# Kernel optimization log

Hardware: AMD Instinct MI355X
Metric: run time of the kernel (lower is better)

Reference implementation:

```python
import jax, jax.numpy as jnp
import numpy as np

N, E = 50000, 800000
IN_DIM, HID, OUT, HEADS = 128, 128, 64, 4
C1 = HID // HEADS  # 32 per-head channels in gat1
NEG_SLOPE = 0.2


def _gat_conv(x, src, dst, W, a_src, a_dst, b, heads, ch):
    """PyG GATConv (inference): gather -> edge attention -> segment softmax -> scatter."""
    n = x.shape[0]
    h = (x @ W).reshape(n, heads, ch)                      # [N,H,C]
    alpha_src = jnp.einsum('nhc,hc->nh', h, a_src)         # [N,H]
    alpha_dst = jnp.einsum('nhc,hc->nh', h, a_dst)         # [N,H]
    e = jax.nn.leaky_relu(alpha_src[src] + alpha_dst[dst], NEG_SLOPE)  # [E,H]
    m = jax.ops.segment_max(e, dst, num_segments=n)        # per-target max (stable softmax)
    e = jnp.exp(e - m[dst])
    denom = jax.ops.segment_sum(e, dst, num_segments=n)
    alpha = e / (denom[dst] + 1e-16)                       # [E,H]
    out = jax.ops.segment_sum(h[src] * alpha[:, :, None], dst, num_segments=n)  # [N,H,C]
    return out.reshape(n, heads * ch) + b


def setup_inputs() -> dict:
    key = jax.random.key(0)
    ks = jax.random.split(key, 16)
    x = jax.random.normal(ks[0], (N, IN_DIM), dtype=jnp.float32)
    edge_index = jax.random.randint(ks[1], (2, E), 0, N, dtype=jnp.int64)
    s = lambda fan_in: 1.0 / np.sqrt(fan_in)
    return {
        'x': x,
        'edge_index': edge_index,
        'W1': jax.random.normal(ks[2], (IN_DIM, HEADS * C1), jnp.float32) * s(IN_DIM),
        'a_src1': jax.random.normal(ks[3], (HEADS, C1), jnp.float32) * s(C1),
        'a_dst1': jax.random.normal(ks[4], (HEADS, C1), jnp.float32) * s(C1),
        'b1': jnp.zeros((HID,), jnp.float32),
        'W2': jax.random.normal(ks[5], (HID, OUT), jnp.float32) * s(HID),
        'a_src2': jax.random.normal(ks[6], (1, OUT), jnp.float32) * s(OUT),
        'a_dst2': jax.random.normal(ks[7], (1, OUT), jnp.float32) * s(OUT),
        'b2': jnp.zeros((OUT,), jnp.float32),
        'pw1': jax.random.normal(ks[8], (OUT, OUT), jnp.float32) * s(OUT),
        'pb1': jnp.zeros((OUT,), jnp.float32),
        'pw2': jax.random.normal(ks[9], (OUT, OUT), jnp.float32) * s(OUT),
        'pb2': jnp.zeros((OUT,), jnp.float32),
    }


def reference(x, edge_index, W1, a_src1, a_dst1, b1, W2, a_src2, a_dst2, b2, pw1, pb1, pw2, pb2):
    n = x.shape[0]
    # PyG GATConv add_self_loops=True
    loops = jnp.arange(n, dtype=edge_index.dtype)
    src = jnp.concatenate([edge_index[0], loops])
    dst = jnp.concatenate([edge_index[1], loops])
    h = jax.nn.elu(_gat_conv(x, src, dst, W1, a_src1, a_dst1, b1, HEADS, C1))
    h = jax.nn.elu(_gat_conv(h, src, dst, W2, a_src2, a_dst2, b2, 1, OUT))
    # origin_proj: Linear -> ReLU -> Linear
    h = jax.nn.relu(h @ pw1 + pb1)
    return h @ pw2 + pb2
```

## Files before the change

### kernel.cpp

```cpp
#include <hip/hip_runtime.h>
#include <math.h>

#define N_NODES 50000
#define N_EDGES 800000
#define ET (N_EDGES + N_NODES)
#define IN_DIM 128
#define HID 128
#define OUT_DIM 64
#define BW 64
#define NBUCK ((N_NODES + BW - 1) / BW)
#define NBLK 256
#define EPB 3328

typedef __attribute__((ext_vector_type(8))) short bf16x8;
typedef __attribute__((ext_vector_type(4))) float f32x4;

__device__ __forceinline__ float lrelu(float x){ return x >= 0.f ? x : 0.2f * x; }
__device__ __forceinline__ float eluf(float x){ return x > 0.f ? x : expm1f(x); }
__device__ __forceinline__ unsigned f2bf(float f){
    unsigned u = __float_as_uint(f);
    return (u + 0x7fffu + ((u >> 16) & 1u)) >> 16;
}
__device__ __forceinline__ float bflo(unsigned u){ return __uint_as_float(u << 16); }
__device__ __forceinline__ float bfhi(unsigned u){ return __uint_as_float(u & 0xffff0000u); }

__global__ __launch_bounds__(256) void k_count(const int* __restrict__ dst, int* __restrict__ C)
{
    __shared__ int cnt[NBUCK];
    const int tid = threadIdx.x, blk = blockIdx.x;
    for (int i = tid; i < NBUCK; i += 256) cnt[i] = 0;
    __syncthreads();
    #pragma unroll
    for (int j = 0; j < EPB / 256; j++) {
        const int e = blk * EPB + j * 256 + tid;
        if (e < ET) {
            const int d = (e < N_EDGES) ? dst[e] : (e - N_EDGES);
            atomicAdd(&cnt[d >> 6], 1);
        }
    }
    __syncthreads();
    for (int b = tid; b < NBUCK; b += 256) C[b * NBLK + blk] = cnt[b];
}

__global__ __launch_bounds__(256) void k_bsumA(const int* __restrict__ C, int* __restrict__ bsum2)
{
    __shared__ int red[4];
    int v = C[blockIdx.x * NBLK + threadIdx.x];
    #pragma unroll
    for (int off = 32; off > 0; off >>= 1) v += __shfl_down(v, off);
    if ((threadIdx.x & 63) == 0) red[threadIdx.x >> 6] = v;
    __syncthreads();
    if (threadIdx.x == 0) bsum2[blockIdx.x] = red[0] + red[1] + red[2] + red[3];
}

__global__ __launch_bounds__(1024) void k_bscanB(const int* __restrict__ bsum2, int* __restrict__ boff2)
{
    __shared__ int part[1024];
    const int t = threadIdx.x;
    int v = (t < NBUCK) ? bsum2[t] : 0;
    part[t] = v;
    __syncthreads();
    #pragma unroll
    for (int d = 1; d < 1024; d <<= 1) {
        int add = (t >= d) ? part[t - d] : 0;
        __syncthreads();
        part[t] += add;
        __syncthreads();
    }
    if (t < NBUCK) boff2[t] = part[t] - v;
    if (t == 0) boff2[NBUCK] = ET;
}

__global__ __launch_bounds__(256) void k_cscanC(const int* __restrict__ C,
                                                const int* __restrict__ boff2,
                                                int* __restrict__ Cs)
{
    __shared__ int part[256];
    const int t = threadIdx.x, b = blockIdx.x;
    int v = C[b * NBLK + t];
    part[t] = v;
    __syncthreads();
    #pragma unroll
    for (int d = 1; d < 256; d <<= 1) {
        int add = (t >= d) ? part[t - d] : 0;
        __syncthreads();
        part[t] += add;
        __syncthreads();
    }
    Cs[b * NBLK + t] = boff2[b] + part[t] - v;
}

__global__ __launch_bounds__(256) void k_part2(const int* __restrict__ src,
                                               const int* __restrict__ dst,
                                               const int* __restrict__ Cs,
                                               uint2* __restrict__ part)
{
    __shared__ int base[NBUCK];
    __shared__ int cnt[NBUCK];
    const int tid = threadIdx.x, blk = blockIdx.x;
    for (int b = tid; b < NBUCK; b += 256) { base[b] = Cs[b * NBLK + blk]; cnt[b] = 0; }
    __syncthreads();
    #pragma unroll
    for (int j = 0; j < EPB / 256; j++) {
        const int e = blk * EPB + j * 256 + tid;
        if (e < ET) {
            int s, d;
            if (e < N_EDGES) { s = src[e]; d = dst[e]; } else { s = d = e - N_EDGES; }
            const int b = d >> 6;
            const int r = atomicAdd(&cnt[b], 1);
            part[base[b] + r] = make_uint2((unsigned)d, (unsigned)s);
        }
    }
}

__global__ __launch_bounds__(256) void k_scat2(const int* __restrict__ boff2,
                                               const uint2* __restrict__ part,
                                               int* __restrict__ rowptr,
                                               int* __restrict__ csr_src)
{
    __shared__ int cnt64[BW];
    __shared__ int nbase[BW];
    const int b = blockIdx.x, tid = threadIdx.x;
    const int n0 = b * BW;
    const int lo = boff2[b], hi = boff2[b + 1];
    if (tid < BW) cnt64[tid] = 0;
    __syncthreads();
    for (int i = lo + tid; i < hi; i += 256) {
        atomicAdd(&cnt64[part[i].x & (BW - 1)], 1);
    }
    __syncthreads();
    if (tid < BW) {
        int v = cnt64[tid];
        int incl = v;
        #pragma unroll
        for (int off = 1; off < 64; off <<= 1) {
            int t2 = __shfl_up(incl, off);
            if (tid >= off) incl += t2;
        }
        const int excl = incl - v;
        nbase[tid] = excl;
        const int n = n0 + tid;
        if (n < N_NODES) rowptr[n] = lo + excl;
        cnt64[tid] = 0;
    }
    if (b == 0 && tid == 0) rowptr[N_NODES] = ET;
    __syncthreads();
    for (int i = lo + tid; i < hi; i += 256) {
        const uint2 p = part[i];
        const int dn = (int)p.x & (BW - 1);
        const int r = atomicAdd(&cnt64[dn], 1);
        csr_src[lo + nbase[dn] + r] = (int)p.y;
    }
}

__global__ __launch_bounds__(256, 2) void k_gemm1(
    const float* __restrict__ x, const float* __restrict__ W1,
    const float* __restrict__ a_s, const float* __restrict__ a_d,
    unsigned* __restrict__ h1b, float* __restrict__ as1, float* __restrict__ ad1)
{
    __shared__ unsigned sWt[128 * 68];
    __shared__ unsigned sxb[64 * 68];
    const int tid = threadIdx.x;
    const int wave = tid >> 6;
    const int lane = tid & 63;
    const int ll   = lane & 15;
    const int quad = lane >> 4;
    const int n0 = blockIdx.x * 64;

    for (int idx = tid; idx < 8192; idx += 256) {
        const int n = idx & 127, kp = idx >> 7;
        const float w0 = W1[(2 * kp) * 128 + n];
        const float w1 = W1[(2 * kp + 1) * 128 + n];
        sWt[n * 68 + kp] = f2bf(w0) | (f2bf(w1) << 16);
    }
    for (int idx = tid; idx < 4096; idx += 256) {
        const int node = idx >> 6, kp = idx & 63;
        const int n = n0 + node;
        unsigned pk = 0;
        if (n < N_NODES) {
            const float x0 = x[n * 128 + 2 * kp];
            const float x1 = x[n * 128 + 2 * kp + 1];
            pk = f2bf(x0) | (f2bf(x1) << 16);
        }
        sxb[node * 68 + kp] = pk;
    }
    __syncthreads();

    f32x4 acc[8];
    #pragma unroll
    for (int t = 0; t < 8; t++) acc[t] = (f32x4){0.f, 0.f, 0.f, 0.f};

    #pragma unroll
    for (int kk = 0; kk < 4; kk++) {
        const int kpo = 16 * kk + 4 * quad;
        const bf16x8 a = *(const bf16x8*)&sxb[(16 * wave + ll) * 68 + kpo];
        #pragma unroll
        for (int t = 0; t < 8; t++) {
            const bf16x8 b = *(const bf16x8*)&sWt[(16 * t + ll) * 68 + kpo];
            acc[t] = __builtin_amdgcn_mfma_f32_16x16x32_bf16(a, b, acc[t], 0, 0, 0);
        }
    }

    float as_v[8], ad_v[8];
    #pragma unroll
    for (int t = 0; t < 8; t++) { as_v[t] = a_s[16 * t + ll]; ad_v[t] = a_d[16 * t + ll]; }
    unsigned short* h1u = (unsigned short*)h1b;
    #pragma unroll
    for (int r = 0; r < 4; r++) {
        const int n = n0 + 16 * wave + 4 * quad + r;
        float ps0 = acc[0][r] * as_v[0] + acc[1][r] * as_v[1];
        float ps1 = acc[2][r] * as_v[2] + acc[3][r] * as_v[3];
        float ps2 = acc[4][r] * as_v[4] + acc[5][r] * as_v[5];
        float ps3 = acc[6][r] * as_v[6] + acc[7][r] * as_v[7];
        float pd0 = acc[0][r] * ad_v[0] + acc[1][r] * ad_v[1];
        float pd1 = acc[2][r] * ad_v[2] + acc[3][r] * ad_v[3];
        float pd2 = acc[4][r] * ad_v[4] + acc[5][r] * ad_v[5];
        float pd3 = acc[6][r] * ad_v[6] + acc[7][r] * ad_v[7];
        #pragma unroll
        for (int off = 1; off < 16; off <<= 1) {
            ps0 += __shfl_xor(ps0, off); ps1 += __shfl_xor(ps1, off);
            ps2 += __shfl_xor(ps2, off); ps3 += __shfl_xor(ps3, off);
            pd0 += __shfl_xor(pd0, off); pd1 += __shfl_xor(pd1, off);
            pd2 += __shfl_xor(pd2, off); pd3 += __shfl_xor(pd3, off);
        }
        if (n < N_NODES) {
            #pragma unroll
            for (int t = 0; t < 8; t++)
                h1u[n * 128 + 16 * t + ll] = (unsigned short)f2bf(acc[t][r]);
            if (ll == 0) {
                as1[n * 4 + 0] = ps0; as1[n * 4 + 1] = ps1;
                as1[n * 4 + 2] = ps2; as1[n * 4 + 3] = ps3;
                ad1[n * 4 + 0] = pd0; ad1[n * 4 + 1] = pd1;
                ad1[n * 4 + 2] = pd2; ad1[n * 4 + 3] = pd3;
            }
        }
    }
}

__global__ __launch_bounds__(256) void k_aggr1(
    const int* __restrict__ rowptr, const int* __restrict__ csr_src,
    const float* __restrict__ as1, const float* __restrict__ ad1,
    const uint4* __restrict__ h1u4, float* __restrict__ acc1)
{
    const int d  = blockIdx.x * 16 + (threadIdx.x >> 4);
    const int c8 = threadIdx.x & 15;
    const int hd = c8 >> 2;
    const int r0 = rowptr[d], r1 = rowptr[d + 1];
    const float adv = ad1[d * 4 + hd];
    float den = 0.f;
    float acc[8];
    #pragma unroll
    for (int m = 0; m < 8; m++) acc[m] = 0.f;
    int i = r0;
    for (; i + 2 <= r1; i += 2) {
        const int s0 = csr_src[i], s1 = csr_src[i + 1];
        const float e0 = as1[s0 * 4 + hd], e1 = as1[s1 * 4 + hd];
        const uint4 u0 = h1u4[s0 * 16 + c8];
        const uint4 u1 = h1u4[s1 * 16 + c8];
        const float w0 = expf(lrelu(e0 + adv));
        const float w1 = expf(lrelu(e1 + adv));
        den += w0 + w1;
        acc[0] = fmaf(bflo(u0.x), w0, acc[0]); acc[1] = fmaf(bfhi(u0.x), w0, acc[1]);
        acc[2] = fmaf(bflo(u0.y), w0, acc[2]); acc[3] = fmaf(bfhi(u0.y), w0, acc[3]);
        acc[4] = fmaf(bflo(u0.z), w0, acc[4]); acc[5] = fmaf(bfhi(u0.z), w0, acc[5]);
        acc[6] = fmaf(bflo(u0.w), w0, acc[6]); acc[7] = fmaf(bfhi(u0.w), w0, acc[7]);
        acc[0] = fmaf(bflo(u1.x), w1, acc[0]); acc[1] = fmaf(bfhi(u1.x), w1, acc[1]);
        acc[2] = fmaf(bflo(u1.y), w1, acc[2]); acc[3] = fmaf(bfhi(u1.y), w1, acc[3]);
        acc[4] = fmaf(bflo(u1.z), w1, acc[4]); acc[5] = fmaf(bfhi(u1.z), w1, acc[5]);
        acc[6] = fmaf(bflo(u1.w), w1, acc[6]); acc[7] = fmaf(bfhi(u1.w), w1, acc[7]);
    }
    if (i < r1) {
        const int s = csr_src[i];
        const float w = expf(lrelu(as1[s * 4 + hd] + adv));
        const uint4 u = h1u4[s * 16 + c8];
        den += w;
        acc[0] = fmaf(bflo(u.x), w, acc[0]); acc[1] = fmaf(bfhi(u.x), w, acc[1]);
        acc[2] = fmaf(bflo(u.y), w, acc[2]); acc[3] = fmaf(bfhi(u.y), w, acc[3]);
        acc[4] = fmaf(bflo(u.z), w, acc[4]); acc[5] = fmaf(bfhi(u.z), w, acc[5]);
        acc[6] = fmaf(bflo(u.w), w, acc[6]); acc[7] = fmaf(bfhi(u.w), w, acc[7]);
    }
    const float inv = 1.f / (den + 1e-16f);
    float4 o0 = make_float4(acc[0] * inv, acc[1] * inv, acc[2] * inv, acc[3] * inv);
    float4 o1 = make_float4(acc[4] * inv, acc[5] * inv, acc[6] * inv, acc[7] * inv);
    ((float4*)acc1)[d * 32 + 2 * c8 + 0] = o0;
    ((float4*)acc1)[d * 32 + 2 * c8 + 1] = o1;
}

__global__ __launch_bounds__(256, 4) void k_layer2(
    const float* __restrict__ acc1, const float* __restrict__ b1,
    const float* __restrict__ W2, const float* __restrict__ a_s2, const float* __restrict__ a_d2,
    unsigned* __restrict__ h2b, float* __restrict__ as2, float* __restrict__ ad2)
{
    __shared__ unsigned sWt[64 * 68];
    __shared__ unsigned sxb[64 * 68];
    const int tid = threadIdx.x;
    const int wave = tid >> 6;
    const int lane = tid & 63;
    const int ll   = lane & 15;
    const int quad = lane >> 4;
    const int n0 = blockIdx.x * 64;

    for (int idx = tid; idx < 4096; idx += 256) {
        const int n = idx & 63, kp = idx >> 6;
        const float w0 = W2[(2 * kp) * 64 + n];
        const float w1 = W2[(2 * kp + 1) * 64 + n];
        sWt[n * 68 + kp] = f2bf(w0) | (f2bf(w1) << 16);
    }
    for (int idx = tid; idx < 4096; idx += 256) {
        const int node = idx >> 6, kp = idx & 63;
        const int n = n0 + node;
        unsigned pk = 0;
        if (n < N_NODES) {
            const float v0 = eluf(acc1[n * 128 + 2 * kp]     + b1[2 * kp]);
            const float v1 = eluf(acc1[n * 128 + 2 * kp + 1] + b1[2 * kp + 1]);
            pk = f2bf(v0) | (f2bf(v1) << 16);
        }
        sxb[node * 68 + kp] = pk;
    }
    __syncthreads();

    f32x4 acc[4];
    #pragma unroll
    for (int t = 0; t < 4; t++) acc[t] = (f32x4){0.f, 0.f, 0.f, 0.f};

    #pragma unroll
    for (int kk = 0; kk < 4; kk++) {
        const int kpo = 16 * kk + 4 * quad;
        const bf16x8 a = *(const bf16x8*)&sxb[(16 * wave + ll) * 68 + kpo];
        #pragma unroll
        for (int t = 0; t < 4; t++) {
            const bf16x8 b = *(const bf16x8*)&sWt[(16 * t + ll) * 68 + kpo];
            acc[t] = __builtin_amdgcn_mfma_f32_16x16x32_bf16(a, b, acc[t], 0, 0, 0);
        }
    }

    float as_v[4], ad_v[4];
    #pragma unroll
    for (int t = 0; t < 4; t++) { as_v[t] = a_s2[16 * t + ll]; ad_v[t] = a_d2[16 * t + ll]; }
    unsigned short* h2u = (unsigned short*)h2b;
    #pragma unroll
    for (int r = 0; r < 4; r++) {
        const int n = n0 + 16 * wave + 4 * quad + r;
        float ps = acc[0][r] * as_v[0] + acc[1][r] * as_v[1]
                 + acc[2][r] * as_v[2] + acc[3][r] * as_v[3];
        float pd = acc[0][r] * ad_v[0] + acc[1][r] * ad_v[1]
                 + acc[2][r] * ad_v[2] + acc[3][r] * ad_v[3];
        #pragma unroll
        for (int off = 1; off < 16; off <<= 1) {
            ps += __shfl_xor(ps, off);
            pd += __shfl_xor(pd, off);
        }
        if (n < N_NODES) {
            #pragma unroll
            for (int t = 0; t < 4; t++)
                h2u[n * 64 + 16 * t + ll] = (unsigned short)f2bf(acc[t][r]);
            if (ll == 0) { as2[n] = ps; ad2[n] = pd; }
        }
    }
}

__global__ __launch_bounds__(256) void k_aggr2(
    const int* __restrict__ rowptr, const int* __restrict__ csr_src,
    const float* __restrict__ as2, const float* __restrict__ ad2,
    const uint4* __restrict__ h2u4, float* __restrict__ acc2)
{
    const int d  = blockIdx.x * 32 + (threadIdx.x >> 3);
    const int c8 = threadIdx.x & 7;
    if (d >= N_NODES) return;
    const int r0 = rowptr[d], r1 = rowptr[d + 1];
    const float adv = ad2[d];
    float den = 0.f;
    float acc[8];
    #pragma unroll
    for (int m = 0; m < 8; m++) acc[m] = 0.f;
    int i = r0;
    for (; i + 2 <= r1; i += 2) {
        const int s0 = csr_src[i], s1 = csr_src[i + 1];
        const float e0 = as2[s0], e1 = as2[s1];
        const uint4 u0 = h2u4[s0 * 8 + c8];
        const uint4 u1 = h2u4[s1 * 8 + c8];
        const float w0 = expf(lrelu(e0 + adv));
        const float w1 = expf(lrelu(e1 + adv));
        den += w0 + w1;
        acc[0] = fmaf(bflo(u0.x), w0, acc[0]); acc[1] = fmaf(bfhi(u0.x), w0, acc[1]);
        acc[2] = fmaf(bflo(u0.y), w0, acc[2]); acc[3] = fmaf(bfhi(u0.y), w0, acc[3]);
        acc[4] = fmaf(bflo(u0.z), w0, acc[4]); acc[5] = fmaf(bfhi(u0.z), w0, acc[5]);
        acc[6] = fmaf(bflo(u0.w), w0, acc[6]); acc[7] = fmaf(bfhi(u0.w), w0, acc[7]);
        acc[0] = fmaf(bflo(u1.x), w1, acc[0]); acc[1] = fmaf(bfhi(u1.x), w1, acc[1]);
        acc[2] = fmaf(bflo(u1.y), w1, acc[2]); acc[3] = fmaf(bfhi(u1.y), w1, acc[3]);
        acc[4] = fmaf(bflo(u1.z), w1, acc[4]); acc[5] = fmaf(bfhi(u1.z), w1, acc[5]);
        acc[6] = fmaf(bflo(u1.w), w1, acc[6]); acc[7] = fmaf(bfhi(u1.w), w1, acc[7]);
    }
    if (i < r1) {
        const int s = csr_src[i];
        const float w = expf(lrelu(as2[s] + adv));
        const uint4 u = h2u4[s * 8 + c8];
        den += w;
        acc[0] = fmaf(bflo(u.x), w, acc[0]); acc[1] = fmaf(bfhi(u.x), w, acc[1]);
        acc[2] = fmaf(bflo(u.y), w, acc[2]); acc[3] = fmaf(bfhi(u.y), w, acc[3]);
        acc[4] = fmaf(bflo(u.z), w, acc[4]); acc[5] = fmaf(bfhi(u.z), w, acc[5]);
        acc[6] = fmaf(bflo(u.w), w, acc[6]); acc[7] = fmaf(bfhi(u.w), w, acc[7]);
    }
    const float inv = 1.f / (den + 1e-16f);
    float4 o0 = make_float4(acc[0] * inv, acc[1] * inv, acc[2] * inv, acc[3] * inv);
    float4 o1 = make_float4(acc[4] * inv, acc[5] * inv, acc[6] * inv, acc[7] * inv);
    ((float4*)acc2)[d * 16 + 2 * c8 + 0] = o0;
    ((float4*)acc2)[d * 16 + 2 * c8 + 1] = o1;
}

__global__ __launch_bounds__(256, 2) void k_out(
    const float* __restrict__ acc2, const float* __restrict__ b2,
    const float* __restrict__ pw1, const float* __restrict__ pb1,
    const float* __restrict__ pw2, const float* __restrict__ pb2,
    float* __restrict__ out)
{
    __shared__ float s1[64 * 64];
    __shared__ float s2[64 * 64];
    __shared__ float so[64][68];
    __shared__ float sp[64][68];
    const int tid = threadIdx.x;
    for (int i = tid; i < 1024; i += 256) {
        ((float4*)s1)[i] = ((const float4*)pw1)[i];
        ((float4*)s2)[i] = ((const float4*)pw2)[i];
    }
    const int cg = tid & 15;
    const int ng = tid >> 4;
    const float4 pb1_4 = ((const float4*)pb1)[cg];
    const float4 pb2_4 = ((const float4*)pb2)[cg];
    const int nGroups = (N_NODES + 63) / 64;
    for (int g = blockIdx.x; g < nGroups; g += gridDim.x) {
        const int n0 = g * 64;
        __syncthreads();
        #pragma unroll
        for (int j = 0; j < 4; j++) {
            const int i = tid + 256 * j;
            const int node = i >> 4, quad = i & 15;
            const int n = n0 + node;
            float4 v = make_float4(0.f, 0.f, 0.f, 0.f);
            if (n < N_NODES) {
                v = ((const float4*)acc2)[n * 16 + quad];
                const float4 bb = ((const float4*)b2)[quad];
                v.x = eluf(v.x + bb.x);
                v.y = eluf(v.y + bb.y);
                v.z = eluf(v.z + bb.z);
                v.w = eluf(v.w + bb.w);
            }
            *(float4*)&so[node][4 * quad] = v;
        }
        __syncthreads();
        float4 p[4];
        #pragma unroll
        for (int m = 0; m < 4; m++) p[m] = pb1_4;
        #pragma unroll 8
        for (int k = 0; k < 64; k++) {
            const float4 w = *(const float4*)&s1[k * 64 + 4 * cg];
            #pragma unroll
            for (int m = 0; m < 4; m++) {
                const float xv = so[4 * ng + m][k];
                p[m].x = fmaf(xv, w.x, p[m].x);
                p[m].y = fmaf(xv, w.y, p[m].y);
                p[m].z = fmaf(xv, w.z, p[m].z);
                p[m].w = fmaf(xv, w.w, p[m].w);
            }
        }
        #pragma unroll
        for (int m = 0; m < 4; m++) {
            p[m].x = fmaxf(p[m].x, 0.f); p[m].y = fmaxf(p[m].y, 0.f);
            p[m].z = fmaxf(p[m].z, 0.f); p[m].w = fmaxf(p[m].w, 0.f);
            *(float4*)&sp[4 * ng + m][4 * cg] = p[m];
        }
        __syncthreads();
        float4 o[4];
        #pragma unroll
        for (int m = 0; m < 4; m++) o[m] = pb2_4;
        #pragma unroll 8
        for (int k = 0; k < 64; k++) {
            const float4 w = *(const float4*)&s2[k * 64 + 4 * cg];
            #pragma unroll
            for (int m = 0; m < 4; m++) {
                const float xv = sp[4 * ng + m][k];
                o[m].x = fmaf(xv, w.x, o[m].x);
                o[m].y = fmaf(xv, w.y, o[m].y);
                o[m].z = fmaf(xv, w.z, o[m].z);
                o[m].w = fmaf(xv, w.w, o[m].w);
            }
        }
        #pragma unroll
        for (int m = 0; m < 4; m++) {
            const int n = n0 + 4 * ng + m;
            if (n < N_NODES) ((float4*)out)[n * 16 + cg] = o[m];
        }
    }
}

extern "C" void kernel_launch(void* const* d_in, const int* in_sizes, int n_in,
                              void* d_out, int out_size, void* d_ws, size_t ws_size,
                              hipStream_t stream)
{
    const float* x      = (const float*)d_in[0];
    const int*   ei     = (const int*)d_in[1];
    const int*   src    = ei;
    const int*   dst    = ei + N_EDGES;
    const float* W1     = (const float*)d_in[2];
    const float* a_src1 = (const float*)d_in[3];
    const float* a_dst1 = (const float*)d_in[4];
    const float* b1     = (const float*)d_in[5];
    const float* W2     = (const float*)d_in[6];
    const float* a_src2 = (const float*)d_in[7];
    const float* a_dst2 = (const float*)d_in[8];
    const float* b2     = (const float*)d_in[9];
    const float* pw1    = (const float*)d_in[10];
    const float* pb1    = (const float*)d_in[11];
    const float* pw2    = (const float*)d_in[12];
    const float* pb2    = (const float*)d_in[13];

    uint2* part  = (uint2*)d_ws;
    int* ibase   = (int*)(part + ET);
    int* rowptr  = ibase;
    int* C       = rowptr + 50001;
    int* Cs      = C + 200192;
    int* bsum2   = Cs + 200192;
    int* boff2   = bsum2 + 782;
    int* csr_src = boff2 + 785;
    unsigned* h1b = (unsigned*)(csr_src + 850000);
    unsigned* h2b = h1b + 3200000;
    float* fws   = (float*)(h2b + 1600000);
    float* as1   = fws;
    float* ad1   = as1 + 200000;
    float* acc1  = ad1 + 200000;
    float* as2   = acc1 + 6400000;
    float* ad2   = as2 + 50000;
    float* acc2  = ad2 + 50000;

    k_count<<<NBLK, 256, 0, stream>>>(dst, C);
    k_bsumA<<<NBUCK, 256, 0, stream>>>(C, bsum2);
    k_bscanB<<<1, 1024, 0, stream>>>(bsum2, boff2);
    k_cscanC<<<NBUCK, 256, 0, stream>>>(C, boff2, Cs);
    k_part2<<<NBLK, 256, 0, stream>>>(src, dst, Cs, part);
    k_scat2<<<NBUCK, 256, 0, stream>>>(boff2, part, rowptr, csr_src);

    k_gemm1<<<(N_NODES + 63) / 64, 256, 0, stream>>>(x, W1, a_src1, a_dst1, h1b, as1, ad1);
    k_aggr1<<<N_NODES / 16, 256, 0, stream>>>(rowptr, csr_src, as1, ad1,
                                              (const uint4*)h1b, acc1);

    k_layer2<<<(N_NODES + 63) / 64, 256, 0, stream>>>(acc1, b1, W2, a_src2, a_dst2, h2b, as2, ad2);
    k_aggr2<<<(N_NODES + 31) / 32, 256, 0, stream>>>(rowptr, csr_src, as2, ad2,
                                                     (const uint4*)h2b, acc2);

    k_out<<<782, 256, 0, stream>>>(acc2, b2, pw1, pb1, pw2, pb2, (float*)d_out);
}
```

Baseline: 247.2 us.

## Fuse GAT aggregation kernels into the following dense transform kernels

Merges layer-1 aggregation with the layer-2 GEMM, and layer-2 aggregation with the output MLP. Each block aggregates its 64 nodes straight into shared memory before the matmul, so the fp32 acc1 and acc2 intermediates no longer go to and from global memory and two launches disappear. In exchange each block now does a longer, irregular gather phase with less parallelism per node (16 or 8 threads loop over 4 or 2 nodes). This may reduce latency hiding, and the new launch bounds of 2 blocks per CU could limit occupancy.

```diff
diff --git a/kernel.cpp b/kernel.cpp
--- a/kernel.cpp
+++ b/kernel.cpp
@@ -237,67 +237,16 @@
     }
 }
 
-__global__ __launch_bounds__(256) void k_aggr1(
+__global__ __launch_bounds__(256, 2) void k_aggr1l2(
     const int* __restrict__ rowptr, const int* __restrict__ csr_src,
     const float* __restrict__ as1, const float* __restrict__ ad1,
-    const uint4* __restrict__ h1u4, float* __restrict__ acc1)
-{
-    const int d  = blockIdx.x * 16 + (threadIdx.x >> 4);
-    const int c8 = threadIdx.x & 15;
-    const int hd = c8 >> 2;
-    const int r0 = rowptr[d], r1 = rowptr[d + 1];
-    const float adv = ad1[d * 4 + hd];
-    float den = 0.f;
-    float acc[8];
-    #pragma unroll
-    for (int m = 0; m < 8; m++) acc[m] = 0.f;
-    int i = r0;
-    for (; i + 2 <= r1; i += 2) {
-        const int s0 = csr_src[i], s1 = csr_src[i + 1];
-        const float e0 = as1[s0 * 4 + hd], e1 = as1[s1 * 4 + hd];
-        const uint4 u0 = h1u4[s0 * 16 + c8];
-        const uint4 u1 = h1u4[s1 * 16 + c8];
-        const float w0 = expf(lrelu(e0 + adv));
-        const float w1 = expf(lrelu(e1 + adv));
-        den += w0 + w1;
-        acc[0] = fmaf(bflo(u0.x), w0, acc[0]); acc[1] = fmaf(bfhi(u0.x), w0, acc[1]);
-        acc[2] = fmaf(bflo(u0.y), w0, acc[2]); acc[3] = fmaf(bfhi(u0.y), w0, acc[3]);
-        acc[4] = fmaf(bflo(u0.z), w0, acc[4]); acc[5] = fmaf(bfhi(u0.z), w0, acc[5]);
-        acc[6] = fmaf(bflo(u0.w), w0, acc[6]); acc[7] = fmaf(bfhi(u0.w), w0, acc[7]);
-        acc[0] = fmaf(bflo(u1.x), w1, acc[0]); acc[1] = fmaf(bfhi(u1.x), w1, acc[1]);
-        acc[2] = fmaf(bflo(u1.y), w1, acc[2]); acc[3] = fmaf(bfhi(u1.y), w1, acc[3]);
-        acc[4] = fmaf(bflo(u1.z), w1, acc[4]); acc[5] = fmaf(bfhi(u1.z), w1, acc[5]);
-        acc[6] = fmaf(bflo(u1.w), w1, acc[6]); acc[7] = fmaf(bfhi(u1.w), w1, acc[7]);
-    }
-    if (i < r1) {
-        const int s = csr_src[i];
-        const float w = expf(lrelu(as1[s * 4 + hd] + adv));
-        const uint4 u = h1u4[s * 16 + c8];
-        den += w;
-        acc[0] = fmaf(bflo(u.x), w, acc[0]); acc[1] = fmaf(bfhi(u.x), w, acc[1]);
-        acc[2] = fmaf(bflo(u.y), w, acc[2]); acc[3] = fmaf(bfhi(u.y), w, acc[3]);
-        acc[4] = fmaf(bflo(u.z), w, acc[4]); acc[5] = fmaf(bfhi(u.z), w, acc[5]);
-        acc[6] = fmaf(bflo(u.w), w, acc[6]); acc[7] = fmaf(bfhi(u.w), w, acc[7]);
-    }
-    const float inv = 1.f / (den + 1e-16f);
-    float4 o0 = make_float4(acc[0] * inv, acc[1] * inv, acc[2] * inv, acc[3] * inv);
-    float4 o1 = make_float4(acc[4] * inv, acc[5] * inv, acc[6] * inv, acc[7] * inv);
-    ((float4*)acc1)[d * 32 + 2 * c8 + 0] = o0;
-    ((float4*)acc1)[d * 32 + 2 * c8 + 1] = o1;
-}
-
-__global__ __launch_bounds__(256, 4) void k_layer2(
-    const float* __restrict__ acc1, const float* __restrict__ b1,
+    const uint4* __restrict__ h1u4, const float* __restrict__ b1,
     const float* __restrict__ W2, const float* __restrict__ a_s2, const float* __restrict__ a_d2,
     unsigned* __restrict__ h2b, float* __restrict__ as2, float* __restrict__ ad2)
 {
     __shared__ unsigned sWt[64 * 68];
     __shared__ unsigned sxb[64 * 68];
     const int tid = threadIdx.x;
-    const int wave = tid >> 6;
-    const int lane = tid & 63;
-    const int ll   = lane & 15;
-    const int quad = lane >> 4;
     const int n0 = blockIdx.x * 64;
 
     for (int idx = tid; idx < 4096; idx += 256) {
@@ -306,23 +255,64 @@
         const float w1 = W2[(2 * kp + 1) * 64 + n];
         sWt[n * 68 + kp] = f2bf(w0) | (f2bf(w1) << 16);
     }
-    for (int idx = tid; idx < 4096; idx += 256) {
-        const int node = idx >> 6, kp = idx & 63;
-        const int n = n0 + node;
-        unsigned pk = 0;
-        if (n < N_NODES) {
-            const float v0 = eluf(acc1[n * 128 + 2 * kp]     + b1[2 * kp]);
-            const float v1 = eluf(acc1[n * 128 + 2 * kp + 1] + b1[2 * kp + 1]);
-            pk = f2bf(v0) | (f2bf(v1) << 16);
-        }
-        sxb[node * 68 + kp] = pk;
-    }
-    __syncthreads();
-
-    f32x4 acc[4];
-    #pragma unroll
-    for (int t = 0; t < 4; t++) acc[t] = (f32x4){0.f, 0.f, 0.f, 0.f};
-
+
+    const int g16 = tid >> 4;
+    const int c8  = tid & 15;
+    const int hd  = c8 >> 2;
+    for (int rep = 0; rep < 4; rep++) {
+        const int node = 4 * g16 + rep;
+        const int d = n0 + node;
+        float den = 0.f;
+        float acc[8];
+        #pragma unroll
+        for (int m = 0; m < 8; m++) acc[m] = 0.f;
+        if (d < N_NODES) {
+            const int r0 = rowptr[d], r1 = rowptr[d + 1];
+            const float adv = ad1[d * 4 + hd];
+            int i = r0;
+            for (; i + 2 <= r1; i += 2) {
+                const int s0 = csr_src[i], s1 = csr_src[i + 1];
+                const float e0 = as1[s0 * 4 + hd], e1 = as1[s1 * 4 + hd];
+                const uint4 u0 = h1u4[s0 * 16 + c8];
+                const uint4 u1 = h1u4[s1 * 16 + c8];
+                const float w0 = expf(lrelu(e0 + adv));
+                const float w1 = expf(lrelu(e1 + adv));
+                den += w0 + w1;
+                acc[0] = fmaf(bflo(u0.x), w0, acc[0]); acc[1] = fmaf(bfhi(u0.x), w0, acc[1]);
+                acc[2] = fmaf(bflo(u0.y), w0, acc[2]); acc[3] = fmaf(bfhi(u0.y), w0, acc[3]);
+                acc[4] = fmaf(bflo(u0.z), w0, acc[4]); acc[5] = fmaf(bfhi(u0.z), w0, acc[5]);
+                acc[6] = fmaf(bflo(u0.w), w0, acc[6]); acc[7] = fmaf(bfhi(u0.w), w0, acc[7]);
+                acc[0] = fmaf(bflo(u1.x), w1, acc[0]); acc[1] = fmaf(bfhi(u1.x), w1, acc[1]);
+                acc[2] = fmaf(bflo(u1.y), w1, acc[2]); acc[3] = fmaf(bfhi(u1.y), w1, acc[3]);
+                acc[4] = fmaf(bflo(u1.z), w1, acc[4]); acc[5] = fmaf(bfhi(u1.z), w1, acc[5]);
+                acc[6] = fmaf(bflo(u1.w), w1, acc[6]); acc[7] = fmaf(bfhi(u1.w), w1, acc[7]);
+            }
+            if (i < r1) {
+                const int s = csr_src[i];
+                const float w = expf(lrelu(as1[s * 4 + hd] + adv));
+                const uint4 u = h1u4[s * 16 + c8];
+                den += w;
+                acc[0] = fmaf(bflo(u.x), w, acc[0]); acc[1] = fmaf(bfhi(u.x), w, acc[1]);
+                acc[2] = fmaf(bflo(u.y), w, acc[2]); acc[3] = fmaf(bfhi(u.y), w, acc[3]);
+                acc[4] = fmaf(bflo(u.z), w, acc[4]); acc[5] = fmaf(bfhi(u.z), w, acc[5]);
+                acc[6] = fmaf(bflo(u.w), w, acc[6]); acc[7] = fmaf(bfhi(u.w), w, acc[7]);
+            }
+        }
+        const float inv = 1.f / (den + 1e-16f);
+        #pragma unroll
+        for (int j = 0; j < 4; j++) {
+            const float v0 = eluf(acc[2 * j]     * inv + b1[8 * c8 + 2 * j]);
+            const float v1 = eluf(acc[2 * j + 1] * inv + b1[8 * c8 + 2 * j + 1]);
+            sxb[node * 68 + 4 * c8 + j] = f2bf(v0) | (f2bf(v1) << 16);
+        }
+    }
+    __syncthreads();
+
+    const int wave = tid >> 6, lane = tid & 63;
+    const int ll = lane & 15, quad = lane >> 4;
+    f32x4 accm[4];
+    #pragma unroll
+    for (int t = 0; t < 4; t++) accm[t] = (f32x4){0.f, 0.f, 0.f, 0.f};
     #pragma unroll
     for (int kk = 0; kk < 4; kk++) {
         const int kpo = 16 * kk + 4 * quad;
@@ -330,10 +320,9 @@
         #pragma unroll
         for (int t = 0; t < 4; t++) {
             const bf16x8 b = *(const bf16x8*)&sWt[(16 * t + ll) * 68 + kpo];
-            acc[t] = __builtin_amdgcn_mfma_f32_16x16x32_bf16(a, b, acc[t], 0, 0, 0);
-        }
-    }
-
+            accm[t] = __builtin_amdgcn_mfma_f32_16x16x32_bf16(a, b, accm[t], 0, 0, 0);
+        }
+    }
     float as_v[4], ad_v[4];
     #pragma unroll
     for (int t = 0; t < 4; t++) { as_v[t] = a_s2[16 * t + ll]; ad_v[t] = a_d2[16 * t + ll]; }
@@ -341,10 +330,10 @@
     #pragma unroll
     for (int r = 0; r < 4; r++) {
         const int n = n0 + 16 * wave + 4 * quad + r;
-        float ps = acc[0][r] * as_v[0] + acc[1][r] * as_v[1]
-                 + acc[2][r] * as_v[2] + acc[3][r] * as_v[3];
-        float pd = acc[0][r] * ad_v[0] + acc[1][r] * ad_v[1]
-                 + acc[2][r] * ad_v[2] + acc[3][r] * ad_v[3];
+        float ps = accm[0][r] * as_v[0] + accm[1][r] * as_v[1]
+                 + accm[2][r] * as_v[2] + accm[3][r] * as_v[3];
+        float pd = accm[0][r] * ad_v[0] + accm[1][r] * ad_v[1]
+                 + accm[2][r] * ad_v[2] + accm[3][r] * ad_v[3];
         #pragma unroll
         for (int off = 1; off < 16; off <<= 1) {
             ps += __shfl_xor(ps, off);
@@ -353,63 +342,16 @@
         if (n < N_NODES) {
             #pragma unroll
             for (int t = 0; t < 4; t++)
-                h2u[n * 64 + 16 * t + ll] = (unsigned short)f2bf(acc[t][r]);
+                h2u[n * 64 + 16 * t + ll] = (unsigned short)f2bf(accm[t][r]);
             if (ll == 0) { as2[n] = ps; ad2[n] = pd; }
         }
     }
 }
 
-__global__ __launch_bounds__(256) void k_aggr2(
+__global__ __launch_bounds__(256, 2) void k_aggr2out(
     const int* __restrict__ rowptr, const int* __restrict__ csr_src,
     const float* __restrict__ as2, const float* __restrict__ ad2,
-    const uint4* __restrict__ h2u4, float* __restrict__ acc2)
-{
-    const int d  = blockIdx.x * 32 + (threadIdx.x >> 3);
-    const int c8 = threadIdx.x & 7;
-    if (d >= N_NODES) return;
-    const int r0 = rowptr[d], r1 = rowptr[d + 1];
-    const float adv = ad2[d];
-    float den = 0.f;
-    float acc[8];
-    #pragma unroll
-    for (int m = 0; m < 8; m++) acc[m] = 0.f;
-    int i = r0;
-    for (; i + 2 <= r1; i += 2) {
-        const int s0 = csr_src[i], s1 = csr_src[i + 1];
-        const float e0 = as2[s0], e1 = as2[s1];
-        const uint4 u0 = h2u4[s0 * 8 + c8];
-        const uint4 u1 = h2u4[s1 * 8 + c8];
-        const float w0 = expf(lrelu(e0 + adv));
-        const float w1 = expf(lrelu(e1 + adv));
-        den += w0 + w1;
-        acc[0] = fmaf(bflo(u0.x), w0, acc[0]); acc[1] = fmaf(bfhi(u0.x), w0, acc[1]);
-        acc[2] = fmaf(bflo(u0.y), w0, acc[2]); acc[3] = fmaf(bfhi(u0.y), w0, acc[3]);
-        acc[4] = fmaf(bflo(u0.z), w0, acc[4]); acc[5] = fmaf(bfhi(u0.z), w0, acc[5]);
-        acc[6] = fmaf(bflo(u0.w), w0, acc[6]); acc[7] = fmaf(bfhi(u0.w), w0, acc[7]);
-        acc[0] = fmaf(bflo(u1.x), w1, acc[0]); acc[1] = fmaf(bfhi(u1.x), w1, acc[1]);
-        acc[2] = fmaf(bflo(u1.y), w1, acc[2]); acc[3] = fmaf(bfhi(u1.y), w1, acc[3]);
-        acc[4] = fmaf(bflo(u1.z), w1, acc[4]); acc[5] = fmaf(bfhi(u1.z), w1, acc[5]);
-        acc[6] = fmaf(bflo(u1.w), w1, acc[6]); acc[7] = fmaf(bfhi(u1.w), w1, acc[7]);
-    }
-    if (i < r1) {
-        const int s = csr_src[i];
-        const float w = expf(lrelu(as2[s] + adv));
-        const uint4 u = h2u4[s * 8 + c8];
-        den += w;
-        acc[0] = fmaf(bflo(u.x), w, acc[0]); acc[1] = fmaf(bfhi(u.x), w, acc[1]);
-        acc[2] = fmaf(bflo(u.y), w, acc[2]); acc[3] = fmaf(bfhi(u.y), w, acc[3]);
-        acc[4] = fmaf(bflo(u.z), w, acc[4]); acc[5] = fmaf(bfhi(u.z), w, acc[5]);
-        acc[6] = fmaf(bflo(u.w), w, acc[6]); acc[7] = fmaf(bfhi(u.w), w, acc[7]);
-    }
-    const float inv = 1.f / (den + 1e-16f);
-    float4 o0 = make_float4(acc[0] * inv, acc[1] * inv, acc[2] * inv, acc[3] * inv);
-    float4 o1 = make_float4(acc[4] * inv, acc[5] * inv, acc[6] * inv, acc[7] * inv);
-    ((float4*)acc2)[d * 16 + 2 * c8 + 0] = o0;
-    ((float4*)acc2)[d * 16 + 2 * c8 + 1] = o1;
-}
-
-__global__ __launch_bounds__(256, 2) void k_out(
-    const float* __restrict__ acc2, const float* __restrict__ b2,
+    const uint4* __restrict__ h2u4, const float* __restrict__ b2,
     const float* __restrict__ pw1, const float* __restrict__ pb1,
     const float* __restrict__ pw2, const float* __restrict__ pb2,
     float* __restrict__ out)
@@ -419,77 +361,105 @@
     __shared__ float so[64][68];
     __shared__ float sp[64][68];
     const int tid = threadIdx.x;
+    const int n0 = blockIdx.x * 64;
     for (int i = tid; i < 1024; i += 256) {
         ((float4*)s1)[i] = ((const float4*)pw1)[i];
         ((float4*)s2)[i] = ((const float4*)pw2)[i];
     }
+
+    const int g8 = tid >> 3;
+    const int c8 = tid & 7;
+    for (int rep = 0; rep < 2; rep++) {
+        const int node = 2 * g8 + rep;
+        const int d = n0 + node;
+        float den = 0.f;
+        float acc[8];
+        #pragma unroll
+        for (int m = 0; m < 8; m++) acc[m] = 0.f;
+        if (d < N_NODES) {
+            const int r0 = rowptr[d], r1 = rowptr[d + 1];
+            const float adv = ad2[d];
+            int i = r0;
+            for (; i + 2 <= r1; i += 2) {
+                const int s0 = csr_src[i], s1v = csr_src[i + 1];
+                const float e0 = as2[s0], e1 = as2[s1v];
+                const uint4 u0 = h2u4[s0 * 8 + c8];
+                const uint4 u1 = h2u4[s1v * 8 + c8];
+                const float w0 = expf(lrelu(e0 + adv));
+                const float w1 = expf(lrelu(e1 + adv));
+                den += w0 + w1;
+                acc[0] = fmaf(bflo(u0.x), w0, acc[0]); acc[1] = fmaf(bfhi(u0.x), w0, acc[1]);
+                acc[2] = fmaf(bflo(u0.y), w0, acc[2]); acc[3] = fmaf(bfhi(u0.y), w0, acc[3]);
+                acc[4] = fmaf(bflo(u0.z), w0, acc[4]); acc[5] = fmaf(bfhi(u0.z), w0, acc[5]);
+                acc[6] = fmaf(bflo(u0.w), w0, acc[6]); acc[7] = fmaf(bfhi(u0.w), w0, acc[7]);
+                acc[0] = fmaf(bflo(u1.x), w1, acc[0]); acc[1] = fmaf(bfhi(u1.x), w1, acc[1]);
+                acc[2] = fmaf(bflo(u1.y), w1, acc[2]); acc[3] = fmaf(bfhi(u1.y), w1, acc[3]);
+                acc[4] = fmaf(bflo(u1.z), w1, acc[4]); acc[5] = fmaf(bfhi(u1.z), w1, acc[5]);
+                acc[6] = fmaf(bflo(u1.w), w1, acc[6]); acc[7] = fmaf(bfhi(u1.w), w1, acc[7]);
+            }
+            if (i < r1) {
+                const int s = csr_src[i];
+                const float w = expf(lrelu(as2[s] + adv));
+                const uint4 u = h2u4[s * 8 + c8];
+                den += w;
+                acc[0] = fmaf(bflo(u.x), w, acc[0]); acc[1] = fmaf(bfhi(u.x), w, acc[1]);
+                acc[2] = fmaf(bflo(u.y), w, acc[2]); acc[3] = fmaf(bfhi(u.y), w, acc[3]);
+                acc[4] = fmaf(bflo(u.z), w, acc[4]); acc[5] = fmaf(bfhi(u.z), w, acc[5]);
+                acc[6] = fmaf(bflo(u.w), w, acc[6]); acc[7] = fmaf(bfhi(u.w), w, acc[7]);
+            }
+        }
+        const float inv = 1.f / (den + 1e-16f);
+        #pragma unroll
+        for (int m = 0; m < 8; m++)
+            so[node][8 * c8 + m] = eluf(acc[m] * inv + b2[8 * c8 + m]);
+    }
+    __syncthreads();
+
     const int cg = tid & 15;
     const int ng = tid >> 4;
     const float4 pb1_4 = ((const float4*)pb1)[cg];
     const float4 pb2_4 = ((const float4*)pb2)[cg];
-    const int nGroups = (N_NODES + 63) / 64;
-    for (int g = blockIdx.x; g < nGroups; g += gridDim.x) {
-        const int n0 = g * 64;
-        __syncthreads();
-        #pragma unroll
-        for (int j = 0; j < 4; j++) {
-            const int i = tid + 256 * j;
-            const int node = i >> 4, quad = i & 15;
-            const int n = n0 + node;
-            float4 v = make_float4(0.f, 0.f, 0.f, 0.f);
-            if (n < N_NODES) {
-                v = ((const float4*)acc2)[n * 16 + quad];
-                const float4 bb = ((const float4*)b2)[quad];
-                v.x = eluf(v.x + bb.x);
-                v.y = eluf(v.y + bb.y);
-                v.z = eluf(v.z + bb.z);
-                v.w = eluf(v.w + bb.w);
-            }
-            *(float4*)&so[node][4 * quad] = v;
-        }
-        __syncthreads();
-        float4 p[4];
-        #pragma unroll
-        for (int m = 0; m < 4; m++) p[m] = pb1_4;
-        #pragma unroll 8
-        for (int k = 0; k < 64; k++) {
-            const float4 w = *(const float4*)&s1[k * 64 + 4 * cg];
-            #pragma unroll
-            for (int m = 0; m < 4; m++) {
-                const float xv = so[4 * ng + m][k];
-                p[m].x = fmaf(xv, w.x, p[m].x);
-                p[m].y = fmaf(xv, w.y, p[m].y);
-                p[m].z = fmaf(xv, w.z, p[m].z);
-                p[m].w = fmaf(xv, w.w, p[m].w);
-            }
-        }
+    float4 p[4];
+    #pragma unroll
+    for (int m = 0; m < 4; m++) p[m] = pb1_4;
+    #pragma unroll 8
+    for (int k = 0; k < 64; k++) {
+        const float4 w = *(const float4*)&s1[k * 64 + 4 * cg];
         #pragma unroll
         for (int m = 0; m < 4; m++) {
-            p[m].x = fmaxf(p[m].x, 0.f); p[m].y = fmaxf(p[m].y, 0.f);
-            p[m].z = fmaxf(p[m].z, 0.f); p[m].w = fmaxf(p[m].w, 0.f);
-            *(float4*)&sp[4 * ng + m][4 * cg] = p[m];
-        }
-        __syncthreads();
-        float4 o[4];
-        #pragma unroll
-        for (int m = 0; m < 4; m++) o[m] = pb2_4;
-        #pragma unroll 8
-        for (int k = 0; k < 64; k++) {
-            const float4 w = *(const float4*)&s2[k * 64 + 4 * cg];
-            #pragma unroll
-            for (int m = 0; m < 4; m++) {
-                const float xv = sp[4 * ng + m][k];
-                o[m].x = fmaf(xv, w.x, o[m].x);
-                o[m].y = fmaf(xv, w.y, o[m].y);
-                o[m].z = fmaf(xv, w.z, o[m].z);
-                o[m].w = fmaf(xv, w.w, o[m].w);
-            }
-        }
+            const float xv = so[4 * ng + m][k];
+            p[m].x = fmaf(xv, w.x, p[m].x);
+            p[m].y = fmaf(xv, w.y, p[m].y);
+            p[m].z = fmaf(xv, w.z, p[m].z);
+            p[m].w = fmaf(xv, w.w, p[m].w);
+        }
+    }
+    #pragma unroll
+    for (int m = 0; m < 4; m++) {
+        p[m].x = fmaxf(p[m].x, 0.f); p[m].y = fmaxf(p[m].y, 0.f);
+        p[m].z = fmaxf(p[m].z, 0.f); p[m].w = fmaxf(p[m].w, 0.f);
+        *(float4*)&sp[4 * ng + m][4 * cg] = p[m];
+    }
+    __syncthreads();
+    float4 o[4];
+    #pragma unroll
+    for (int m = 0; m < 4; m++) o[m] = pb2_4;
+    #pragma unroll 8
+    for (int k = 0; k < 64; k++) {
+        const float4 w = *(const float4*)&s2[k * 64 + 4 * cg];
         #pragma unroll
         for (int m = 0; m < 4; m++) {
-            const int n = n0 + 4 * ng + m;
-            if (n < N_NODES) ((float4*)out)[n * 16 + cg] = o[m];
-        }
+            const float xv = sp[4 * ng + m][k];
+            o[m].x = fmaf(xv, w.x, o[m].x);
+            o[m].y = fmaf(xv, w.y, o[m].y);
+            o[m].z = fmaf(xv, w.z, o[m].z);
+            o[m].w = fmaf(xv, w.w, o[m].w);
+        }
+    }
+    #pragma unroll
+    for (int m = 0; m < 4; m++) {
+        const int n = n0 + 4 * ng + m;
+        if (n < N_NODES) ((float4*)out)[n * 16 + cg] = o[m];
     }
 }
 
@@ -527,10 +497,8 @@
     float* fws   = (float*)(h2b + 1600000);
     float* as1   = fws;
     float* ad1   = as1 + 200000;
-    float* acc1  = ad1 + 200000;
-    float* as2   = acc1 + 6400000;
+    float* as2   = ad1 + 200000;
     float* ad2   = as2 + 50000;
-    float* acc2  = ad2 + 50000;
 
     k_count<<<NBLK, 256, 0, stream>>>(dst, C);
     k_bsumA<<<NBUCK, 256, 0, stream>>>(C, bsum2);
@@ -540,12 +508,14 @@
     k_scat2<<<NBUCK, 256, 0, stream>>>(boff2, part, rowptr, csr_src);
 
     k_gemm1<<<(N_NODES + 63) / 64, 256, 0, stream>>>(x, W1, a_src1, a_dst1, h1b, as1, ad1);
-    k_aggr1<<<N_NODES / 16, 256, 0, stream>>>(rowptr, csr_src, as1, ad1,
-                                              (const uint4*)h1b, acc1);
-
-    k_layer2<<<(N_NODES + 63) / 64, 256, 0, stream>>>(acc1, b1, W2, a_src2, a_dst2, h2b, as2, ad2);
-    k_aggr2<<<(N_NODES + 31) / 32, 256, 0, stream>>>(rowptr, csr_src, as2, ad2,
-                                                     (const uint4*)h2b, acc2);
-
-    k_out<<<782, 256, 0, stream>>>(acc2, b2, pw1, pb1, pw2, pb2, (float*)d_out);
-}
+
+    k_aggr1l2<<<(N_NODES + 63) / 64, 256, 0, stream>>>(rowptr, csr_src, as1, ad1,
+                                                       (const uint4*)h1b, b1,
+                                                       W2, a_src2, a_dst2,
+                                                       h2b, as2, ad2);
+
+    k_aggr2out<<<(N_NODES + 63) / 64, 256, 0, stream>>>(rowptr, csr_src, as2, ad2,
+                                                        (const uint4*)h2b, b2,
+                                                        pw1, pb1, pw2, pb2,
+                                                        (float*)d_out);
+}
```

Result: slower. 272.9 us (+10.4%).
